# Kernel tuning notes

Measured on AMD Instinct MI355X. Metric: run time of the kernel, lower is better.

Reference implementation:

```python
import jax, jax.numpy as jnp
import numpy as np

B, C, W = 32, 128, 4096          # batch, channel (= emb_dim = D), window/input_dim
HID = [2048, 1024, 512]          # encoder hidden dims (last dim transforms)
K, D = 512, 128                  # codebook: K = hidden_dims[-1], D = emb_dim
BETA = 0.25


def setup_inputs() -> dict:
    key = jax.random.key(0)
    ks = jax.random.split(key, 12)
    def lin(k, fan_in, fan_out):
        return jax.random.normal(k, (fan_in, fan_out), jnp.float32) * (1.0 / np.sqrt(fan_in))
    inp = {"x": jax.random.normal(ks[0], (B, C, W), jnp.float32)}
    edims = [W] + HID  # 4096 -> 2048 -> 1024 -> 512
    for i in range(3):
        inp[f"ew{i}"] = lin(ks[1 + i], edims[i], edims[i + 1])
        inp[f"eb{i}"] = jnp.zeros((edims[i + 1],), jnp.float32)
    inp["codebook"] = jax.random.uniform(ks[4], (K, D), jnp.float32, -1.0 / K, 1.0 / K)
    ddims = [512, 1024, 2048, 4096]  # decoder mirrors encoder
    for i in range(3):
        inp[f"dw{i}"] = lin(ks[5 + i], ddims[i], ddims[i + 1])
        inp[f"db{i}"] = jnp.zeros((ddims[i + 1],), jnp.float32)
    return inp


def reference(x, ew0, eb0, ew1, eb1, ew2, eb2, codebook, dw0, db0, dw1, db1, dw2, db2):
    # ---- encoder: LinearBlock = Linear + ReLU over last dim ----
    h = x
    for wgt, b in ((ew0, eb0), (ew1, eb1), (ew2, eb2)):
        h = jax.nn.relu(h @ wgt + b)            # [B, C, L] with L shrinking to 512

    # ---- VectorQuantizer1d ----
    lat = jnp.swapaxes(h, 1, 2)                 # [B, L, D]
    flat = lat.reshape(-1, D)                   # [B*L, D]
    # cdist^2 via expansion, then argmin -> nearest-codebook lookup
    dist = (jnp.sum(flat * flat, axis=1, keepdims=True)
            + jnp.sum(codebook * codebook, axis=1)
            - 2.0 * flat @ codebook.T)          # [B*L, K]
    inds = jnp.argmin(dist, axis=1)             # [B*L]
    q = codebook[inds].reshape(lat.shape)       # one-hot matmul == gather

    commit = jnp.mean((jax.lax.stop_gradient(q) - lat) ** 2)
    embed = jnp.mean((q - jax.lax.stop_gradient(lat)) ** 2)
    vq_loss = BETA * commit + embed

    q_st = lat + jax.lax.stop_gradient(q - lat)  # straight-through estimator
    z = jnp.swapaxes(q_st, 1, 2)                 # back to [B, D, L]

    # ---- decoder: Linear+ReLU blocks, last block has no activation ----
    for i, (wgt, b) in enumerate(((dw0, db0), (dw1, db1), (dw2, db2))):
        z = z @ wgt + b
        if i < 2:
            z = jax.nn.relu(z)
    return z, x, vq_loss
```

## Files before the change

### kernel.cpp

```cpp
#include <hip/hip_runtime.h>


typedef _Float16 f16;
typedef _Float16 f16x8 __attribute__((ext_vector_type(8)));
typedef _Float16 f16x4 __attribute__((ext_vector_type(4)));
typedef float    f32x4 __attribute__((ext_vector_type(4)));

typedef const unsigned int __attribute__((address_space(1)))* gp1_t;
typedef unsigned int __attribute__((address_space(3)))*       lp3_t;

__device__ __forceinline__ void gl_lds16(const void* g, void* l) {
  __builtin_amdgcn_global_load_lds((gp1_t)g, (lp3_t)l, 16, 0, 0);
}

#define BATCH 32
#define CDIM  128
#define WDIM  4096
#define LDIM  512
#define KCB   512
#define DCB   128

#define SX    128.0f
#define SW    256.0f
#define SA    256.0f
#define SCB   4096.0f
#define SQ    4096.0f


#define G8_SRC(t, As, Bs, kk) \
  const f16 *As, *Bs; int kk; \
  { int ts_ = (t) < NT ? (t) : NT - 1; int kg_ = ts_ << 6; \
    if (SPLIT) { int sg_ = (kg_ >= 2 * K) ? 2 : ((kg_ >= K) ? 1 : 0); \
      kk = kg_ - sg_ * K; As = (sg_ == 2) ? Al : Ah; Bs = (sg_ == 1) ? Bl : Bh; } \
    else { As = Ah; Bs = Bh; kk = kg_; } }

#define G8_STAGE(src, row0, kk, off) \
  _Pragma("unroll") \
  for (int j_ = 0; j_ < 2; ++j_) { \
    const int p_ = j_ * 8192 + tid * 16; \
    const int r_ = p_ >> 7; \
    const int c_ = (p_ >> 4) & 7; \
    gl_lds16((src) + (size_t)((row0) + r_) * K + (kk) + ((c_ ^ (r_ & 7)) << 3), \
             smem + (off) + p_); \
  }

#define G8_STAGE_A(t, u) do { G8_SRC(t, As_, Bs_, kk_) \
  G8_STAGE(As_, m0 + (u) * 128, kk_, ((t) & 1) * ASZ + (u) * 16384) } while (0)
#define G8_STAGE_B(t, u) do { G8_SRC(t, As_, Bs_, kk_) \
  G8_STAGE(Bs_, n0 + (u) * 128, kk_, BBASE + ((t) & 1) * BSZ + (u) * 16384) } while (0)

#define G8_READ_A(buf, mh) \
  _Pragma("unroll") \
  for (int m_ = 0; m_ < MR2; ++m_) { \
    const int r_ = wr * (MR * 16) + ((mh) * MR2 + m_) * 16 + fr; \
    _Pragma("unroll") \
    for (int ks_ = 0; ks_ < 2; ++ks_) \
      ar[m_][ks_] = *(const f16x8*)(smem + (buf) * ASZ + r_ * 128 + \
                                    ((((ks_ << 2) + hq) ^ (r_ & 7)) << 4)); \
  }

#define G8_READ_B(buf, nh, br) \
  _Pragma("unroll") \
  for (int n_ = 0; n_ < 2; ++n_) { \
    const int r_ = wc * 64 + ((nh) * 2 + n_) * 16 + fr; \
    _Pragma("unroll") \
    for (int ks_ = 0; ks_ < 2; ++ks_) \
      br[n_][ks_] = *(const f16x8*)(smem + BBASE + (buf) * BSZ + r_ * 128 + \
                                    ((((ks_ << 2) + hq) ^ (r_ & 7)) << 4)); \
  }

#define G8_MFMA(mh, nh, br) \
  _Pragma("unroll") \
  for (int m_ = 0; m_ < MR2; ++m_) \
  _Pragma("unroll") \
  for (int n_ = 0; n_ < 2; ++n_) \
  _Pragma("unroll") \
  for (int ks_ = 0; ks_ < 2; ++ks_) \
    acc[(mh) * MR2 + m_][(nh) * 2 + n_] = __builtin_amdgcn_mfma_f32_16x16x32_f16( \
        ar[m_][ks_], br[n_][ks_], acc[(mh) * MR2 + m_][(nh) * 2 + n_], 0, 0, 0);

#define G8_BAR() do { asm volatile("" ::: "memory"); \
  __builtin_amdgcn_s_barrier(); asm volatile("" ::: "memory"); } while (0)
#define G8_LGKM0() do { asm volatile("s_waitcnt lgkmcnt(0)" ::: "memory"); \
  __builtin_amdgcn_sched_barrier(0); } while (0)
#define G8_VMGATE() do { \
  if constexpr (BUNITS == 2) asm volatile("s_waitcnt vmcnt(4)" ::: "memory"); \
  else                       asm volatile("s_waitcnt vmcnt(2)" ::: "memory"); } while (0)
#define G8_PRIO1() __builtin_amdgcn_s_setprio(1)
#define G8_PRIO0() __builtin_amdgcn_s_setprio(0)

template<int SPLIT, int EPI, int WM, int WN, int MR>
__global__ __launch_bounds__(512, 2)
void vq_gemm8(const f16* __restrict__ Ah, const f16* __restrict__ Al,
              const f16* __restrict__ Bh, const f16* __restrict__ Bl,
              const float* __restrict__ bias,
              void* __restrict__ Co, void* __restrict__ Co2,
              int M, int N, int K, float unscale, float outscale)
{
  constexpr int MR2 = MR / 2;
  constexpr int GBM = WM * MR * 16;
  constexpr int GBN = WN * 64;
  constexpr int BUNITS = GBN / 128;
  constexpr int ASZ = GBM * 128;
  constexpr int BSZ = GBN * 128;
  constexpr int BBASE = 2 * ASZ;
  constexpr int LDSZ = 2 * ASZ + 2 * BSZ;

  __shared__ __align__(16) char smem[LDSZ];

  const int tid = threadIdx.x;
  const int lane = tid & 63;
  const int w = tid >> 6;
  const int wr = w / WN, wc = w % WN;
  const int fr = lane & 15, hq = lane >> 4;

  const int nbx = N / GBN;
  const int cpx = gridDim.x >> 3;
  const int swz = ((int)blockIdx.x & 7) * cpx + ((int)blockIdx.x >> 3);
  const int bx = swz % nbx, by = swz / nbx;
  const int m0 = by * GBM, n0 = bx * GBN;

  const int NT = (SPLIT ? 3 * K : K) >> 6;
  const int NI = NT >> 1;

  f32x4 acc[MR][4] = {};
  f16x8 ar[MR2][2], br0[2][2], br1[2][2];

  G8_STAGE_B(0, 0); if constexpr (BUNITS == 2) G8_STAGE_B(0, 1);
  G8_STAGE_A(0, 0); G8_STAGE_A(0, 1);
  G8_STAGE_B(1, 0); if constexpr (BUNITS == 2) G8_STAGE_B(1, 1);

  for (int i = 0; i < NI; ++i) {
    const int to = 2 * i + 1, te = 2 * i + 2, to2 = 2 * i + 3;
    if constexpr (BUNITS == 1) {
      G8_VMGATE(); G8_BAR();
      G8_READ_A(0, 0) G8_READ_B(0, 0, br0) G8_READ_B(0, 1, br1)
      G8_STAGE_A(to, 0); G8_STAGE_A(to, 1);
      G8_BAR(); G8_LGKM0();
      G8_PRIO1(); G8_MFMA(0, 0, br0) G8_MFMA(0, 1, br1) G8_PRIO0();
      G8_BAR();
      G8_READ_A(0, 1)
      G8_STAGE_B(te, 0);
      G8_BAR(); G8_LGKM0();
      G8_PRIO1(); G8_MFMA(1, 0, br0) G8_MFMA(1, 1, br1) G8_PRIO0();
      G8_VMGATE(); G8_BAR();
      G8_READ_A(1, 0) G8_READ_B(1, 0, br0) G8_READ_B(1, 1, br1)
      G8_STAGE_A(te, 0); G8_STAGE_A(te, 1);
      G8_BAR(); G8_LGKM0();
      G8_PRIO1(); G8_MFMA(0, 0, br0) G8_MFMA(0, 1, br1) G8_PRIO0();
      G8_BAR();
      G8_READ_A(1, 1)
      G8_STAGE_B(to2, 0);
      G8_BAR(); G8_LGKM0();
      G8_PRIO1(); G8_MFMA(1, 0, br0) G8_MFMA(1, 1, br1) G8_PRIO0();
    } else {
      G8_VMGATE(); G8_BAR();
      G8_READ_A(0, 0) G8_READ_B(0, 0, br0)
      G8_STAGE_A(to, 0);
      G8_BAR(); G8_LGKM0(); G8_PRIO1(); G8_MFMA(0, 0, br0) G8_PRIO0();
      G8_BAR();
      G8_READ_B(0, 1, br1)
      G8_STAGE_A(to, 1);
      G8_BAR(); G8_LGKM0(); G8_PRIO1(); G8_MFMA(0, 1, br1) G8_PRIO0();
      G8_BAR();
      G8_READ_A(0, 1)
      G8_STAGE_B(te, 0);
      G8_BAR(); G8_LGKM0(); G8_PRIO1(); G8_MFMA(1, 0, br0) G8_PRIO0();
      G8_BAR();
      G8_STAGE_B(te, 1);
      G8_BAR(); G8_PRIO1(); G8_MFMA(1, 1, br1) G8_PRIO0();
      G8_VMGATE(); G8_BAR();
      G8_READ_A(1, 0) G8_READ_B(1, 0, br0)
      G8_STAGE_A(te, 0);
      G8_BAR(); G8_LGKM0(); G8_PRIO1(); G8_MFMA(0, 0, br0) G8_PRIO0();
      G8_BAR();
      G8_READ_B(1, 1, br1)
      G8_STAGE_A(te, 1);
      G8_BAR(); G8_LGKM0(); G8_PRIO1(); G8_MFMA(0, 1, br1) G8_PRIO0();
      G8_BAR();
      G8_READ_A(1, 1)
      G8_STAGE_B(to2, 0);
      G8_BAR(); G8_LGKM0(); G8_PRIO1(); G8_MFMA(1, 0, br0) G8_PRIO0();
      G8_BAR();
      G8_STAGE_B(to2, 1);
      G8_BAR(); G8_PRIO1(); G8_MFMA(1, 1, br1) G8_PRIO0();
    }
  }

  const int r4 = hq * 4;
#pragma unroll
  for (int mi = 0; mi < MR; ++mi) {
#pragma unroll
    for (int ni = 0; ni < 4; ++ni) {
      const int col = n0 + wc * 64 + ni * 16 + fr;
      const float bv = (EPI == 0) ? 0.f : bias[col];
#pragma unroll
      for (int j = 0; j < 4; ++j) {
        const int row = m0 + wr * (MR * 16) + mi * 16 + r4 + j;
        float y = acc[mi][ni][j] * unscale;
        if (EPI != 0) y += bv;
        if (EPI == 1 || EPI == 2) y = fmaxf(y, 0.f);
        const size_t idx = (size_t)row * N + col;
        if (EPI == 0 || EPI == 3) ((float*)Co)[idx] = y;
        else {
          const float ys = y * outscale;
          const f16 hv = (f16)ys;
          ((f16*)Co)[idx] = hv;
          if (EPI == 1) ((f16*)Co2)[idx] = (f16)(ys - (float)hv);
        }
      }
    }
  }
}

#define BM 128
#define BN 128
#define BK 32

template<int SPLIT, int EPI>
__global__ __launch_bounds__(256, 2)
void vq_gemm(const f16* __restrict__ Ah, const f16* __restrict__ Al,
             const f16* __restrict__ Bh, const f16* __restrict__ Bl,
             const float* __restrict__ bias,
             void* __restrict__ Co, void* __restrict__ Co2,
             int M, int N, int K, float unscale, float outscale)
{
  __shared__ __align__(16) f16 sAh[BM * BK];
  __shared__ __align__(16) f16 sBh[BN * BK];
  __shared__ __align__(16) f16 sAl[SPLIT ? BM * BK : 8];
  __shared__ __align__(16) f16 sBl[SPLIT ? BN * BK : 8];

  const int tid  = threadIdx.x;
  const int lane = tid & 63;
  const int w    = tid >> 6;
  const int nb   = N / BN;
  const int bx   = blockIdx.x % nb;
  const int by   = blockIdx.x / nb;
  const int m0   = by * BM, n0 = bx * BN;
  const int wr   = w >> 1, wc = w & 1;
  const int fr   = lane & 15;
  const int ko   = (lane >> 4) * 8;

  f32x4 acc[4][4] = {};

  const int srow = lane >> 2;
  const int skb  = (lane & 3) * 8;

  for (int k0 = 0; k0 < K; k0 += BK) {
#pragma unroll
    for (int i = 0; i < 2; ++i) {
      const int c  = w * 2 + i;
      const size_t ga = (size_t)(m0 + c * 16 + srow) * K + k0 + skb;
      const size_t gb = (size_t)(n0 + c * 16 + srow) * K + k0 + skb;
      gl_lds16(Ah + ga, &sAh[c * 512]);
      gl_lds16(Bh + gb, &sBh[c * 512]);
      if (SPLIT) {
        gl_lds16(Al + ga, &sAl[c * 512]);
        gl_lds16(Bl + gb, &sBl[c * 512]);
      }
    }
    __syncthreads();

    f16x8 ah[4], bh[4], al[4], bl[4];
#pragma unroll
    for (int mi = 0; mi < 4; ++mi) {
      const int r = (wr * 64 + mi * 16 + fr) * BK + ko;
      ah[mi] = *(const f16x8*)&sAh[r];
      if (SPLIT) al[mi] = *(const f16x8*)&sAl[r];
    }
#pragma unroll
    for (int ni = 0; ni < 4; ++ni) {
      const int r = (wc * 64 + ni * 16 + fr) * BK + ko;
      bh[ni] = *(const f16x8*)&sBh[r];
      if (SPLIT) bl[ni] = *(const f16x8*)&sBl[r];
    }
#pragma unroll
    for (int mi = 0; mi < 4; ++mi)
#pragma unroll
      for (int ni = 0; ni < 4; ++ni) {
        acc[mi][ni] = __builtin_amdgcn_mfma_f32_16x16x32_f16(ah[mi], bh[ni], acc[mi][ni], 0, 0, 0);
        if (SPLIT) {
          acc[mi][ni] = __builtin_amdgcn_mfma_f32_16x16x32_f16(ah[mi], bl[ni], acc[mi][ni], 0, 0, 0);
          acc[mi][ni] = __builtin_amdgcn_mfma_f32_16x16x32_f16(al[mi], bh[ni], acc[mi][ni], 0, 0, 0);
        }
      }
    __syncthreads();
  }

  const int r4 = (lane >> 4) * 4;
#pragma unroll
  for (int mi = 0; mi < 4; ++mi) {
#pragma unroll
    for (int ni = 0; ni < 4; ++ni) {
      const int col = n0 + wc * 64 + ni * 16 + fr;
      const float bv = (EPI == 0) ? 0.0f : bias[col];
#pragma unroll
      for (int j = 0; j < 4; ++j) {
        const int row = m0 + wr * 64 + mi * 16 + r4 + j;
        float y = acc[mi][ni][j] * unscale;
        if (EPI != 0) y += bv;
        if (EPI == 1 || EPI == 2) y = fmaxf(y, 0.0f);
        const size_t idx = (size_t)row * N + col;
        if (EPI == 0 || EPI == 3) {
          ((float*)Co)[idx] = y;
        } else {
          const float ys = y * outscale;
          const f16 hv = (f16)ys;
          ((f16*)Co)[idx] = hv;
          if (EPI == 1) ((f16*)Co2)[idx] = (f16)(ys - (float)hv);
        }
      }
    }
  }
}

__global__ void vq_split(const float* __restrict__ in, f16* __restrict__ hi,
                         f16* __restrict__ lo, int n4, float scale,
                         float* __restrict__ raw)
{
  const int i = blockIdx.x * 256 + threadIdx.x;
  if (i >= n4) return;
  const float4 v = ((const float4*)in)[i];
  if (raw) ((float4*)raw)[i] = v;
  f16x4 h, l;
#pragma unroll
  for (int j = 0; j < 4; ++j) {
    const float s = (&v.x)[j] * scale;
    const f16 hh = (f16)s;
    h[j] = hh;
    l[j] = (f16)(s - (float)hh);
  }
  *(f16x4*)&hi[i * 4] = h;
  *(f16x4*)&lo[i * 4] = l;
}

template<int WRITE_LO>
__global__ void vq_tsplit(const float* __restrict__ W, f16* __restrict__ Th,
                          f16* __restrict__ Tl, int K, int N, float scale)
{
  __shared__ float t[32][33];
  const int n0 = blockIdx.x * 32, k0 = blockIdx.y * 32;
  const int tx = threadIdx.x & 31, ty = threadIdx.x >> 5;
#pragma unroll
  for (int i = 0; i < 4; ++i)
    t[ty + i * 8][tx] = W[(size_t)(k0 + ty + i * 8) * N + n0 + tx];
  __syncthreads();
#pragma unroll
  for (int i = 0; i < 4; ++i) {
    const int n = n0 + ty + i * 8;
    const float v = t[tx][ty + i * 8] * scale;
    const f16 hv = (f16)v;
    Th[(size_t)n * K + k0 + tx] = hv;
    if (WRITE_LO) Tl[(size_t)n * K + k0 + tx] = (f16)(v - (float)hv);
  }
}

__global__ void vq_tpose(const f16* __restrict__ Hh, const f16* __restrict__ Hl,
                         f16* __restrict__ Fh, f16* __restrict__ Fl)
{
  __shared__ f16 th[32][33];
  __shared__ f16 tl[32][33];
  const int bidx = blockIdx.x;
  const int b = bidx >> 6, rem = bidx & 63;
  const int l0 = (rem >> 2) * 32, c0 = (rem & 3) * 32;
  const int tx = threadIdx.x & 31, ty = threadIdx.x >> 5;
  const size_t hbase = (size_t)b * CDIM * LDIM;
#pragma unroll
  for (int i = 0; i < 4; ++i) {
    const int c = c0 + ty + i * 8;
    th[ty + i * 8][tx] = Hh[hbase + (size_t)c * LDIM + l0 + tx];
    tl[ty + i * 8][tx] = Hl[hbase + (size_t)c * LDIM + l0 + tx];
  }
  __syncthreads();
  const size_t fbase = (size_t)b * LDIM * DCB;
#pragma unroll
  for (int i = 0; i < 4; ++i) {
    const int l = l0 + ty + i * 8;
    Fh[fbase + (size_t)l * DCB + c0 + tx] = th[tx][ty + i * 8];
    Fl[fbase + (size_t)l * DCB + c0 + tx] = tl[tx][ty + i * 8];
  }
}

__global__ void vq_cbnorm(const float* __restrict__ cb, float* __restrict__ cbn)
{
  const int k = blockIdx.x * 256 + threadIdx.x;
  if (k >= KCB) return;
  float s = 0.f;
  for (int c = 0; c < DCB; ++c) { const float v = cb[k * DCB + c]; s += v * v; }
  cbn[k] = s;
}

__global__ void vq_argmin(const float* __restrict__ G, const float* __restrict__ cbn,
                          int* __restrict__ inds)
{
  const int row = blockIdx.x;
  const int lane = threadIdx.x;
  const float* g = G + (size_t)row * KCB;
  float best = 1e30f; int bi = 0;
#pragma unroll
  for (int j = 0; j < 8; ++j) {
    const int k = j * 64 + lane;
    const float d = cbn[k] - 2.0f * g[k];
    if (d < best) { best = d; bi = k; }
  }
  for (int off = 32; off; off >>= 1) {
    const float ov = __shfl_xor(best, off);
    const int oi = __shfl_xor(bi, off);
    if (ov < best || (ov == best && oi < bi)) { best = ov; bi = oi; }
  }
  if (lane == 0) inds[row] = bi;
}

__global__ void vq_gather(const float* __restrict__ cb, const int* __restrict__ inds,
                          f16* __restrict__ z0)
{
  const int t = blockIdx.x * 256 + threadIdx.x;
  const int l = t & 511, c = (t >> 9) & 127, b = t >> 16;
  const int ind = inds[b * LDIM + l];
  z0[t] = (f16)(cb[ind * DCB + c] * SQ);
}

__global__ void vq_loss(const f16* __restrict__ Fh, const f16* __restrict__ Fl,
                        const float* __restrict__ cb, const int* __restrict__ inds,
                        float* __restrict__ partials)
{
  const int gw = (blockIdx.x * 256 + threadIdx.x) >> 6;
  const int lane = threadIdx.x & 63;
  float s = 0.f;
  for (int r = gw; r < BATCH * LDIM; r += 1024) {
    const int ind = inds[r];
    const f16* fh = Fh + (size_t)r * DCB;
    const f16* fl = Fl + (size_t)r * DCB;
    const float* q = cb + (size_t)ind * DCB;
#pragma unroll
    for (int j = 0; j < 2; ++j) {
      const int c = j * 64 + lane;
      const float lat = ((float)fh[c] + (float)fl[c]) * (1.0f / SA);
      const float d = q[c] - lat;
      s += d * d;
    }
  }
  for (int off = 32; off; off >>= 1) s += __shfl_xor(s, off);
  __shared__ float wsum[4];
  if (lane == 0) wsum[threadIdx.x >> 6] = s;
  __syncthreads();
  if (threadIdx.x == 0) partials[blockIdx.x] = wsum[0] + wsum[1] + wsum[2] + wsum[3];
}

__global__ void vq_loss_final(const float* __restrict__ partials, float* __restrict__ out)
{
  float s = partials[threadIdx.x];
  for (int off = 32; off; off >>= 1) s += __shfl_xor(s, off);
  __shared__ float wsum[4];
  if ((threadIdx.x & 63) == 0) wsum[threadIdx.x >> 6] = s;
  __syncthreads();
  if (threadIdx.x == 0)
    out[0] = (wsum[0] + wsum[1] + wsum[2] + wsum[3]) * (1.25f / (float)(BATCH * LDIM * DCB));
}

extern "C" void kernel_launch(void* const* d_in, const int* in_sizes, int n_in,
                              void* d_out, int out_size, void* d_ws, size_t ws_size,
                              hipStream_t stream)
{
  const float* x   = (const float*)d_in[0];
  const float* ew0 = (const float*)d_in[1];
  const float* eb0 = (const float*)d_in[2];
  const float* ew1 = (const float*)d_in[3];
  const float* eb1 = (const float*)d_in[4];
  const float* ew2 = (const float*)d_in[5];
  const float* eb2 = (const float*)d_in[6];
  const float* cb  = (const float*)d_in[7];
  const float* dw0 = (const float*)d_in[8];
  const float* db0 = (const float*)d_in[9];
  const float* dw1 = (const float*)d_in[10];
  const float* db1 = (const float*)d_in[11];
  const float* dw2 = (const float*)d_in[12];
  const float* db2 = (const float*)d_in[13];
  float* out = (float*)d_out;

  constexpr size_t N_X  = 4096ull * 4096;
  constexpr size_t N_E0 = 4096ull * 2048, N_E1 = 2048ull * 1024, N_E2 = 1024ull * 512;
  constexpr size_t N_CB = 512ull * 128;
  constexpr size_t N_D0 = 512ull * 1024, N_D1 = 1024ull * 2048, N_D2 = 2048ull * 4096;
  constexpr size_t N_H0 = 4096ull * 2048, N_H1 = 4096ull * 1024, N_H2 = 4096ull * 512;
  constexpr size_t N_FL = 16384ull * 128;
  constexpr size_t N_Z1 = 4096ull * 1024;

  constexpr size_t O_EW0H = 0;
  constexpr size_t O_EW0L = O_EW0H + N_E0 * 2;
  constexpr size_t O_EW1H = O_EW0L + N_E0 * 2;
  constexpr size_t O_EW1L = O_EW1H + N_E1 * 2;
  constexpr size_t O_EW2H = O_EW1L + N_E1 * 2;
  constexpr size_t O_EW2L = O_EW2H + N_E2 * 2;
  constexpr size_t O_CBH  = O_EW2L + N_E2 * 2;
  constexpr size_t O_CBL  = O_CBH + N_CB * 2;
  constexpr size_t O_DW0  = O_CBL + N_CB * 2;
  constexpr size_t O_DW1  = O_DW0 + N_D0 * 2;
  constexpr size_t O_DW2  = O_DW1 + N_D1 * 2;
  constexpr size_t O_XH   = O_DW2 + N_D2 * 2;
  constexpr size_t O_XL   = O_XH + N_X * 2;
  constexpr size_t O_H0H  = O_XL + N_X * 2;
  constexpr size_t O_H0L  = O_H0H + N_H0 * 2;
  constexpr size_t O_H1H  = O_H0L + N_H0 * 2;
  constexpr size_t O_H1L  = O_H1H + N_H1 * 2;
  constexpr size_t O_H2H  = O_H1L + N_H1 * 2;
  constexpr size_t O_H2L  = O_H2H + N_H2 * 2;
  constexpr size_t O_FLH  = O_H2L + N_H2 * 2;
  constexpr size_t O_FLL  = O_FLH + N_FL * 2;
  constexpr size_t O_G    = O_XH;
  constexpr size_t O_INDS = O_XL;
  constexpr size_t O_CBN  = O_XL + (1ull << 17);
  constexpr size_t O_PART = O_XL + (1ull << 18);
  constexpr size_t O_Z0   = O_XL + (1ull << 20);
  constexpr size_t O_ZH1  = O_Z0 + N_H2 * 2;
  constexpr size_t O_ZH2  = O_ZH1 + N_Z1 * 2;

  char* ws = (char*)d_ws;
  f16*   XH = (f16*)(ws + O_XH);   f16* XL = (f16*)(ws + O_XL);
  f16* EW0H = (f16*)(ws + O_EW0H); f16* EW0L = (f16*)(ws + O_EW0L);
  f16* EW1H = (f16*)(ws + O_EW1H); f16* EW1L = (f16*)(ws + O_EW1L);
  f16* EW2H = (f16*)(ws + O_EW2H); f16* EW2L = (f16*)(ws + O_EW2L);
  f16*  CBH = (f16*)(ws + O_CBH);  f16* CBL = (f16*)(ws + O_CBL);
  f16*  DW0 = (f16*)(ws + O_DW0);  f16* DW1 = (f16*)(ws + O_DW1);  f16* DW2 = (f16*)(ws + O_DW2);
  f16*  H0H = (f16*)(ws + O_H0H);  f16* H0L = (f16*)(ws + O_H0L);
  f16*  H1H = (f16*)(ws + O_H1H);  f16* H1L = (f16*)(ws + O_H1L);
  f16*  H2H = (f16*)(ws + O_H2H);  f16* H2L = (f16*)(ws + O_H2L);
  f16*  FLH = (f16*)(ws + O_FLH);  f16* FLL = (f16*)(ws + O_FLL);
  float*  G = (float*)(ws + O_G);
  int* INDS = (int*)(ws + O_INDS);
  float* CBN = (float*)(ws + O_CBN);
  float* PART = (float*)(ws + O_PART);
  f16*   Z0 = (f16*)(ws + O_Z0);
  f16*  ZH1 = (f16*)(ws + O_ZH1);
  f16*  ZH2 = (f16*)(ws + O_ZH2);

  vq_split<<<(int)(N_X / 4 / 256), 256, 0, stream>>>(x, XH, XL, (int)(N_X / 4), SX,
                                                     out + 16777216);
  vq_split<<<(int)(N_CB / 4 / 256), 256, 0, stream>>>(cb, CBH, CBL, (int)(N_CB / 4), SCB,
                                                      nullptr);
  vq_tsplit<1><<<dim3(2048 / 32, 4096 / 32), 256, 0, stream>>>(ew0, EW0H, EW0L, 4096, 2048, SW);
  vq_tsplit<1><<<dim3(1024 / 32, 2048 / 32), 256, 0, stream>>>(ew1, EW1H, EW1L, 2048, 1024, SW);
  vq_tsplit<1><<<dim3(512 / 32, 1024 / 32), 256, 0, stream>>>(ew2, EW2H, EW2L, 1024, 512, SW);
  vq_tsplit<0><<<dim3(1024 / 32, 512 / 32), 256, 0, stream>>>(dw0, DW0, nullptr, 512, 1024, SW);
  vq_tsplit<0><<<dim3(2048 / 32, 1024 / 32), 256, 0, stream>>>(dw1, DW1, nullptr, 1024, 2048, SW);
  vq_tsplit<0><<<dim3(4096 / 32, 2048 / 32), 256, 0, stream>>>(dw2, DW2, nullptr, 2048, 4096, SW);

  vq_gemm8<1, 1, 4, 2, 4><<<256, 512, 0, stream>>>(
      XH, XL, EW0H, EW0L, eb0, H0H, H0L, 4096, 2048, 4096, 1.0f / (SX * SW), SA);
  vq_gemm<1, 1><<<(4096 / BM) * (1024 / BN), 256, 0, stream>>>(
      H0H, H0L, EW1H, EW1L, eb1, H1H, H1L, 4096, 1024, 2048, 1.0f / (SA * SW), SA);
  vq_gemm<1, 1><<<(4096 / BM) * (512 / BN), 256, 0, stream>>>(
      H1H, H1L, EW2H, EW2L, eb2, H2H, H2L, 4096, 512, 1024, 1.0f / (SA * SW), SA);

  vq_tpose<<<BATCH * 64, 256, 0, stream>>>(H2H, H2L, FLH, FLL);
  vq_gemm<1, 0><<<(16384 / BM) * (512 / BN), 256, 0, stream>>>(
      FLH, FLL, CBH, CBL, nullptr, G, nullptr, 16384, 512, 128, 1.0f / (SA * SCB), 0.f);
  vq_cbnorm<<<2, 256, 0, stream>>>(cb, CBN);
  vq_argmin<<<16384, 64, 0, stream>>>(G, CBN, INDS);
  vq_gather<<<(BATCH * CDIM * LDIM) / 256, 256, 0, stream>>>(cb, INDS, Z0);
  vq_loss<<<256, 256, 0, stream>>>(FLH, FLL, cb, INDS, PART);
  vq_loss_final<<<1, 256, 0, stream>>>(PART, out + 33554432);

  vq_gemm<0, 2><<<(4096 / BM) * (1024 / BN), 256, 0, stream>>>(
      Z0, nullptr, DW0, nullptr, db0, ZH1, nullptr, 4096, 1024, 512, 1.0f / (SQ * SW), SQ);
  vq_gemm8<0, 2, 4, 2, 4><<<256, 512, 0, stream>>>(
      ZH1, nullptr, DW1, nullptr, db1, ZH2, nullptr, 4096, 2048, 1024, 1.0f / (SQ * SW), SQ);
  vq_gemm8<0, 3, 2, 4, 8><<<256, 512, 0, stream>>>(
      ZH2, nullptr, DW2, nullptr, db2, out, nullptr, 4096, 4096, 2048, 1.0f / (SQ * SW), 0.f);

  (void)in_sizes; (void)n_in; (void)out_size; (void)ws_size;
}
```

Before: 549.7 us.

## Triple-buffer A tiles in GEMM main loop for deeper prefetch when BUNITS==1

For the BUNITS==1 GEMM configuration, the A operand now uses three LDS buffers instead of two, and the loop is restructured to iterate per k-tile. Each step prefetches tile t+2 and waits with vmcnt(6). The aim is to raise the prefetch distance so global-to-LDS loads are better hidden behind MFMA work. In exchange it uses more LDS per block, which may lower occupancy, and adds rotating buffer-index arithmetic in the loop.

Result: no change. 559.3 us (+1.7%).

```diff
diff --git a/kernel.cpp b/kernel.cpp
--- a/kernel.cpp
+++ b/kernel.cpp
@@ -43,6 +43,11 @@
     gl_lds16((src) + (size_t)((row0) + r_) * K + (kk) + ((c_ ^ (r_ & 7)) << 3), \
              smem + (off) + p_); \
   }
+
+#define GD_STAGE_A(t, u, ab) do { G8_SRC(t, As_, Bs_, kk_) \
+  G8_STAGE(As_, m0 + (u) * 128, kk_, (ab) * ASZ + (u) * 16384) } while (0)
+#define GD_STAGE_B(t, bb) do { G8_SRC(t, As_, Bs_, kk_) \
+  G8_STAGE(Bs_, n0, kk_, BBASE + (bb) * BSZ) } while (0)
 
 #define G8_STAGE_A(t, u) do { G8_SRC(t, As_, Bs_, kk_) \
   G8_STAGE(As_, m0 + (u) * 128, kk_, ((t) & 1) * ASZ + (u) * 16384) } while (0)
@@ -83,9 +88,6 @@
   __builtin_amdgcn_s_barrier(); asm volatile("" ::: "memory"); } while (0)
 #define G8_LGKM0() do { asm volatile("s_waitcnt lgkmcnt(0)" ::: "memory"); \
   __builtin_amdgcn_sched_barrier(0); } while (0)
-#define G8_VMGATE() do { \
-  if constexpr (BUNITS == 2) asm volatile("s_waitcnt vmcnt(4)" ::: "memory"); \
-  else                       asm volatile("s_waitcnt vmcnt(2)" ::: "memory"); } while (0)
 #define G8_PRIO1() __builtin_amdgcn_s_setprio(1)
 #define G8_PRIO0() __builtin_amdgcn_s_setprio(0)
 
@@ -103,8 +105,9 @@
   constexpr int BUNITS = GBN / 128;
   constexpr int ASZ = GBM * 128;
   constexpr int BSZ = GBN * 128;
-  constexpr int BBASE = 2 * ASZ;
-  constexpr int LDSZ = 2 * ASZ + 2 * BSZ;
+  constexpr int NABUF = (BUNITS == 1) ? 3 : 2;
+  constexpr int BBASE = NABUF * ASZ;
+  constexpr int LDSZ = NABUF * ASZ + 2 * BSZ;
 
   __shared__ __align__(16) char smem[LDSZ];
 
@@ -121,40 +124,37 @@
   const int m0 = by * GBM, n0 = bx * GBN;
 
   const int NT = (SPLIT ? 3 * K : K) >> 6;
-  const int NI = NT >> 1;
 
   f32x4 acc[MR][4] = {};
   f16x8 ar[MR2][2], br0[2][2], br1[2][2];
 
-  G8_STAGE_B(0, 0); if constexpr (BUNITS == 2) G8_STAGE_B(0, 1);
-  G8_STAGE_A(0, 0); G8_STAGE_A(0, 1);
-  G8_STAGE_B(1, 0); if constexpr (BUNITS == 2) G8_STAGE_B(1, 1);
-
-  for (int i = 0; i < NI; ++i) {
-    const int to = 2 * i + 1, te = 2 * i + 2, to2 = 2 * i + 3;
-    if constexpr (BUNITS == 1) {
-      G8_VMGATE(); G8_BAR();
-      G8_READ_A(0, 0) G8_READ_B(0, 0, br0) G8_READ_B(0, 1, br1)
-      G8_STAGE_A(to, 0); G8_STAGE_A(to, 1);
+  if constexpr (BUNITS == 1) {
+    GD_STAGE_A(0, 0, 0); GD_STAGE_A(0, 1, 0); GD_STAGE_B(0, 0);
+    GD_STAGE_A(1, 0, 1); GD_STAGE_A(1, 1, 1); GD_STAGE_B(1, 1);
+    int ab = 0, bb = 0;
+    for (int t = 0; t < NT; ++t) {
+      int ab2 = ab + 2; if (ab2 >= 3) ab2 -= 3;
+      asm volatile("s_waitcnt vmcnt(6)" ::: "memory");
+      G8_BAR();
+      G8_READ_A(ab, 0) G8_READ_B(bb, 0, br0) G8_READ_B(bb, 1, br1)
+      GD_STAGE_A(t + 2, 0, ab2); GD_STAGE_A(t + 2, 1, ab2);
       G8_BAR(); G8_LGKM0();
       G8_PRIO1(); G8_MFMA(0, 0, br0) G8_MFMA(0, 1, br1) G8_PRIO0();
       G8_BAR();
-      G8_READ_A(0, 1)
-      G8_STAGE_B(te, 0);
+      G8_READ_A(ab, 1)
+      GD_STAGE_B(t + 2, bb);
       G8_BAR(); G8_LGKM0();
       G8_PRIO1(); G8_MFMA(1, 0, br0) G8_MFMA(1, 1, br1) G8_PRIO0();
-      G8_VMGATE(); G8_BAR();
-      G8_READ_A(1, 0) G8_READ_B(1, 0, br0) G8_READ_B(1, 1, br1)
-      G8_STAGE_A(te, 0); G8_STAGE_A(te, 1);
-      G8_BAR(); G8_LGKM0();
-      G8_PRIO1(); G8_MFMA(0, 0, br0) G8_MFMA(0, 1, br1) G8_PRIO0();
-      G8_BAR();
-      G8_READ_A(1, 1)
-      G8_STAGE_B(to2, 0);
-      G8_BAR(); G8_LGKM0();
-      G8_PRIO1(); G8_MFMA(1, 0, br0) G8_MFMA(1, 1, br1) G8_PRIO0();
-    } else {
-      G8_VMGATE(); G8_BAR();
+      ab = (ab == 2) ? 0 : ab + 1; bb ^= 1;
+    }
+  } else {
+    const int NI = NT >> 1;
+    G8_STAGE_B(0, 0); G8_STAGE_B(0, 1);
+    G8_STAGE_A(0, 0); G8_STAGE_A(0, 1);
+    G8_STAGE_B(1, 0); G8_STAGE_B(1, 1);
+    for (int i = 0; i < NI; ++i) {
+      const int to = 2 * i + 1, te = 2 * i + 2, to2 = 2 * i + 3;
+      asm volatile("s_waitcnt vmcnt(4)" ::: "memory"); G8_BAR();
       G8_READ_A(0, 0) G8_READ_B(0, 0, br0)
       G8_STAGE_A(to, 0);
       G8_BAR(); G8_LGKM0(); G8_PRIO1(); G8_MFMA(0, 0, br0) G8_PRIO0();
@@ -169,7 +169,7 @@
       G8_BAR();
       G8_STAGE_B(te, 1);
       G8_BAR(); G8_PRIO1(); G8_MFMA(1, 1, br1) G8_PRIO0();
-      G8_VMGATE(); G8_BAR();
+      asm volatile("s_waitcnt vmcnt(4)" ::: "memory"); G8_BAR();
       G8_READ_A(1, 0) G8_READ_B(1, 0, br0)
       G8_STAGE_A(te, 0);
       G8_BAR(); G8_LGKM0(); G8_PRIO1(); G8_MFMA(0, 0, br0) G8_PRIO0();
```

## Split-K the first two encoder GEMMs with a separate reduction kernel

Applied to the files above, without the earlier changes.

Adds a split-K mode to the 512-thread GEMM. Each grid.y slice covers a contiguous range of k-tiles and writes fp32 partials into a slab held in the output buffer. A new reduction kernel sums the slices and applies bias, ReLU, scaling and the hi/lo fp16 split. Encoder layers 0 and 1 now use this path with a 256x256 tile config instead of the single-pass kernels, which gives more blocks and better load balance on the 256-CU part. The cost is extra fp32 partial-slab traffic and one more kernel launch per layer.

New measurement: 540.7 us. Within noise of the previous version (-1.6%).

```diff
diff --git a/kernel.cpp b/kernel.cpp
--- a/kernel.cpp
+++ b/kernel.cpp
@@ -29,7 +29,7 @@
 
 #define G8_SRC(t, As, Bs, kk) \
   const f16 *As, *Bs; int kk; \
-  { int ts_ = (t) < NT ? (t) : NT - 1; int kg_ = ts_ << 6; \
+  { int ts_ = (t) < NTloc ? (t) : NTloc - 1; int kg_ = (t0 + ts_) << 6; \
     if (SPLIT) { int sg_ = (kg_ >= 2 * K) ? 2 : ((kg_ >= K) ? 1 : 0); \
       kk = kg_ - sg_ * K; As = (sg_ == 2) ? Al : Ah; Bs = (sg_ == 1) ? Bl : Bh; } \
     else { As = Ah; Bs = Bh; kk = kg_; } }
@@ -95,7 +95,7 @@
               const f16* __restrict__ Bh, const f16* __restrict__ Bl,
               const float* __restrict__ bias,
               void* __restrict__ Co, void* __restrict__ Co2,
-              int M, int N, int K, float unscale, float outscale)
+              int M, int N, int K, int NTloc, float unscale, float outscale)
 {
   constexpr int MR2 = MR / 2;
   constexpr int GBM = WM * MR * 16;
@@ -115,13 +115,13 @@
   const int fr = lane & 15, hq = lane >> 4;
 
   const int nbx = N / GBN;
-  const int cpx = gridDim.x >> 3;
+  const int cpx = (int)gridDim.x >> 3;
   const int swz = ((int)blockIdx.x & 7) * cpx + ((int)blockIdx.x >> 3);
   const int bx = swz % nbx, by = swz / nbx;
   const int m0 = by * GBM, n0 = bx * GBN;
-
-  const int NT = (SPLIT ? 3 * K : K) >> 6;
-  const int NI = NT >> 1;
+  const int t0 = (int)blockIdx.y * NTloc;
+
+  const int NI = NTloc >> 1;
 
   f32x4 acc[MR][4] = {};
   f16x8 ar[MR2][2], br0[2][2], br1[2][2];
@@ -187,20 +187,22 @@
     }
   }
 
+  float* Pslab = (EPI == 4) ? ((float*)Co + (size_t)blockIdx.y * M * N) : nullptr;
   const int r4 = hq * 4;
 #pragma unroll
   for (int mi = 0; mi < MR; ++mi) {
 #pragma unroll
     for (int ni = 0; ni < 4; ++ni) {
       const int col = n0 + wc * 64 + ni * 16 + fr;
-      const float bv = (EPI == 0) ? 0.f : bias[col];
+      const float bv = (EPI == 0 || EPI == 4) ? 0.f : bias[col];
 #pragma unroll
       for (int j = 0; j < 4; ++j) {
         const int row = m0 + wr * (MR * 16) + mi * 16 + r4 + j;
+        const size_t idx = (size_t)row * N + col;
         float y = acc[mi][ni][j] * unscale;
+        if (EPI == 4) { Pslab[idx] = y; continue; }
         if (EPI != 0) y += bv;
         if (EPI == 1 || EPI == 2) y = fmaxf(y, 0.f);
-        const size_t idx = (size_t)row * N + col;
         if (EPI == 0 || EPI == 3) ((float*)Co)[idx] = y;
         else {
           const float ys = y * outscale;
@@ -211,6 +213,33 @@
       }
     }
   }
+}
+
+template<int NS>
+__global__ void vq_ksum(const float* __restrict__ P, const float* __restrict__ bias,
+                        f16* __restrict__ Oh, f16* __restrict__ Ol,
+                        int MN, int N, float unscale, float outscale)
+{
+  const int i4 = (blockIdx.x * 256 + threadIdx.x) * 4;
+  if (i4 >= MN) return;
+  float4 s = ((const float4*)P)[i4 >> 2];
+#pragma unroll
+  for (int sl = 1; sl < NS; ++sl) {
+    const float4 v = ((const float4*)(P + (size_t)sl * MN))[i4 >> 2];
+    s.x += v.x; s.y += v.y; s.z += v.z; s.w += v.w;
+  }
+  const int col = i4 % N;
+  f16x4 h, l;
+#pragma unroll
+  for (int j = 0; j < 4; ++j) {
+    float y = (&s.x)[j] * unscale + bias[col + j];
+    y = fmaxf(y, 0.f) * outscale;
+    const f16 hv = (f16)y;
+    h[j] = hv;
+    l[j] = (f16)(y - (float)hv);
+  }
+  *(f16x4*)&Oh[i4] = h;
+  *(f16x4*)&Ol[i4] = l;
 }
 
 #define BM 128
@@ -533,6 +562,7 @@
   f16*   Z0 = (f16*)(ws + O_Z0);
   f16*  ZH1 = (f16*)(ws + O_ZH1);
   f16*  ZH2 = (f16*)(ws + O_ZH2);
+  float* PSL = out;
 
   vq_split<<<(int)(N_X / 4 / 256), 256, 0, stream>>>(x, XH, XL, (int)(N_X / 4), SX,
                                                      out + 16777216);
@@ -545,10 +575,14 @@
   vq_tsplit<0><<<dim3(2048 / 32, 1024 / 32), 256, 0, stream>>>(dw1, DW1, nullptr, 1024, 2048, SW);
   vq_tsplit<0><<<dim3(4096 / 32, 2048 / 32), 256, 0, stream>>>(dw2, DW2, nullptr, 2048, 4096, SW);
 
-  vq_gemm8<1, 1, 4, 2, 4><<<256, 512, 0, stream>>>(
-      XH, XL, EW0H, EW0L, eb0, H0H, H0L, 4096, 2048, 4096, 1.0f / (SX * SW), SA);
-  vq_gemm<1, 1><<<(4096 / BM) * (1024 / BN), 256, 0, stream>>>(
-      H0H, H0L, EW1H, EW1L, eb1, H1H, H1L, 4096, 1024, 2048, 1.0f / (SA * SW), SA);
+  vq_gemm8<1, 4, 2, 4, 8><<<dim3(128, 2), 512, 0, stream>>>(
+      XH, XL, EW0H, EW0L, nullptr, PSL, nullptr, 4096, 2048, 4096, 96, 1.0f, 0.f);
+  vq_ksum<2><<<(int)(N_H0 / 4 / 256), 256, 0, stream>>>(
+      PSL, eb0, H0H, H0L, (int)N_H0, 2048, 1.0f / (SX * SW), SA);
+  vq_gemm8<1, 4, 2, 4, 8><<<dim3(64, 4), 512, 0, stream>>>(
+      H0H, H0L, EW1H, EW1L, nullptr, PSL, nullptr, 4096, 1024, 2048, 24, 1.0f, 0.f);
+  vq_ksum<4><<<(int)(N_H1 / 4 / 256), 256, 0, stream>>>(
+      PSL, eb1, H1H, H1L, (int)N_H1, 1024, 1.0f / (SA * SW), SA);
   vq_gemm<1, 1><<<(4096 / BM) * (512 / BN), 256, 0, stream>>>(
       H1H, H1L, EW2H, EW2L, eb2, H2H, H2L, 4096, 512, 1024, 1.0f / (SA * SW), SA);
 
@@ -563,10 +597,10 @@
 
   vq_gemm<0, 2><<<(4096 / BM) * (1024 / BN), 256, 0, stream>>>(
       Z0, nullptr, DW0, nullptr, db0, ZH1, nullptr, 4096, 1024, 512, 1.0f / (SQ * SW), SQ);
-  vq_gemm8<0, 2, 4, 2, 4><<<256, 512, 0, stream>>>(
-      ZH1, nullptr, DW1, nullptr, db1, ZH2, nullptr, 4096, 2048, 1024, 1.0f / (SQ * SW), SQ);
-  vq_gemm8<0, 3, 2, 4, 8><<<256, 512, 0, stream>>>(
-      ZH2, nullptr, DW2, nullptr, db2, out, nullptr, 4096, 4096, 2048, 1.0f / (SQ * SW), 0.f);
+  vq_gemm8<0, 2, 4, 2, 4><<<dim3(256, 1), 512, 0, stream>>>(
+      ZH1, nullptr, DW1, nullptr, db1, ZH2, nullptr, 4096, 2048, 1024, 16, 1.0f / (SQ * SW), SQ);
+  vq_gemm8<0, 3, 2, 4, 8><<<dim3(256, 1), 512, 0, stream>>>(
+      ZH2, nullptr, DW2, nullptr, db2, out, nullptr, 4096, 4096, 2048, 32, 1.0f / (SQ * SW), 0.f);
 
   (void)in_sizes; (void)n_in; (void)out_size; (void)ws_size;
 }
```
